# Kernel optimization log

Measured on AMD Instinct MI355X. Metric: run time of the kernel, lower is better.

## Reference

```python
import jax, jax.numpy as jnp
from jax import lax
import numpy as np

BETA = 0.9   # snn.Leaky(beta=0.9)
THR = 1.0    # snntorch default threshold, reset_mechanism='subtract'

@jax.custom_vjp
def spike(x):
    return (x > 0.0).astype(x.dtype)

def _spike_fwd(x):
    return spike(x), x

def _spike_bwd(x, g):
    # snntorch surrogate.atan (alpha=2): dS/dx = 1 / (1 + (pi*x)^2)
    return (g / (1.0 + (jnp.pi * x) ** 2),)

spike.defvjp(_spike_fwd, _spike_bwd)

def lif(inp, mem):
    # snntorch Leaky: reset based on PREVIOUS mem, detached; subtract mechanism
    reset = lax.stop_gradient(spike(mem - THR))
    mem = BETA * mem + inp - reset * THR
    return spike(mem - THR), mem

def conv1d(x, w, b):
    # x: (B, Cin, L), w: (Cout, Cin, K), VALID padding
    y = lax.conv_general_dilated(x, w, window_strides=(1,), padding='VALID',
                                 dimension_numbers=('NCH', 'OIH', 'NCH'))
    return y + b[None, :, None]

def setup_inputs() -> dict:
    key = jax.random.key(0)
    ks = jax.random.split(key, 11)
    B, L, T, num_c = 1024, 30, 100, 10
    def init(k, shape, fan_in):
        bound = 1.0 / np.sqrt(fan_in)
        return jax.random.uniform(k, shape, jnp.float32, -bound, bound)
    return {
        'x':   jax.random.normal(ks[0], (B, 1, L, T), jnp.float32),
        'w1':  init(ks[1], (16, 1, 7), 1 * 7),   'b1': init(ks[2], (16,), 7),
        'w2':  init(ks[3], (32, 16, 5), 16 * 5), 'b2': init(ks[4], (32,), 80),
        'w3':  init(ks[5], (64, 32, 3), 32 * 3), 'b3': init(ks[6], (64,), 96),
        'fw1': init(ks[7], (256, 64 * 18), 64 * 18), 'fb1': init(ks[8], (256,), 64 * 18),
        'fw2': init(ks[9], (num_c, 256), 256),       'fb2': init(ks[10], (num_c,), 256),
    }

def reference(x, w1, b1, w2, b2, w3, b3, fw1, fb1, fw2, fb2):
    B = x.shape[0]
    num_c = fw2.shape[0]
    xt_seq = jnp.transpose(x, (3, 0, 1, 2))  # (T, B, 1, 30)
    mems = (jnp.zeros((B, 16, 24), x.dtype),  # after conv1 (k=7): 30->24
            jnp.zeros((B, 32, 20), x.dtype),  # after conv2 (k=5): 24->20
            jnp.zeros((B, 64, 18), x.dtype),  # after conv3 (k=3): 20->18
            jnp.zeros((B, 256), x.dtype),
            jnp.zeros((B, num_c), x.dtype))
    def step(mems, xt):
        m1, m2, m3, m4, m5 = mems
        h = conv1d(xt, w1, b1); s, m1 = lif(h, m1)
        h = conv1d(s, w2, b2);  s, m2 = lif(h, m2)
        h = conv1d(s, w3, b3);  s, m3 = lif(h, m3)
        h = s.reshape(B, -1) @ fw1.T + fb1; s, m4 = lif(h, m4)
        h = s @ fw2.T + fb2;               s, m5 = lif(h, m5)
        return (m1, m2, m3, m4, m5), s
    _, spk_rec = lax.scan(step, mems, xt_seq)
    return spk_rec  # (T, B, num_c) -- matches torch.stack(spk_rec)
```

## Files before the change

kernel.cpp:

```cpp
#include <hip/hip_runtime.h>
#include <stdint.h>

#define BETA 0.9f

__global__ void transpose_fw1(const float* __restrict__ A, float* __restrict__ At) {
    __shared__ float tile[32][33];
    const int i0 = blockIdx.x * 32;
    const int j0 = blockIdx.y * 32;
    const int tx = threadIdx.x, ty = threadIdx.y;
    for (int r = ty; r < 32; r += 8)
        tile[r][tx] = A[(j0 + r) * 1152 + i0 + tx];
    __syncthreads();
    for (int r = ty; r < 32; r += 8)
        At[(i0 + r) * 256 + j0 + tx] = tile[tx][r];
}

__global__ __launch_bounds__(768, 6) void snn_main(
    const float* __restrict__ x,
    const float* __restrict__ w1, const float* __restrict__ b1,
    const float* __restrict__ w2, const float* __restrict__ b2,
    const float* __restrict__ w3, const float* __restrict__ b3,
    const float* __restrict__ fw1T,
    const float* __restrict__ fb1,
    const float* __restrict__ fw2, const float* __restrict__ fb2,
    float* __restrict__ out)
{
    const int b    = blockIdx.x;
    const int tid  = threadIdx.x;
    const int e    = (tid >= 384) ? 1 : 0;
    const int tl   = tid - 384 * e;
    const int lane = tid & 63;
    const int ew   = tl >> 6;

    __shared__ float w2L[16 * 5 * 32];
    __shared__ float w3L[32 * 3 * 64];
    __shared__ float pacc[2][6][256];
    __shared__ float s1e[2][16 * 24 + 8];
    __shared__ float s4[2][256];
    __shared__ unsigned long long masks[2][18];
    __shared__ unsigned int rm1[2][2][16];
    __shared__ unsigned int cm2[2][2][20];

    const int c1 = tl & 15;
    const int l1 = tl >> 4;
    const int c2 = tl & 31;
    const int g2 = tl >> 5;
    const int l02 = (g2 < 8) ? 2 * g2 : 16 + (g2 - 8);
    const int nl2 = (g2 < 8) ? 2 : 1;
    const int c3 = lane;
    const int l03 = ew * 3;
    const unsigned wmask2 = (ew < 4)  ? (0xFFu << (4 * ew)) :
                            (ew == 4) ? 0x3F0000u :
                                        0xFC0000u;

    for (int i = tid; i < 16 * 5 * 32; i += 768) {
        const int cc = i & 31, r = i >> 5;
        w2L[i] = w2[cc * 80 + r];
    }
    for (int i = tid; i < 32 * 3 * 64; i += 768) {
        const int cc = i & 63, r = i >> 6;
        w3L[i] = w3[cc * 96 + r];
    }
    if (tl < 16) { rm1[e][0][tl] = 0u; rm1[e][1][tl] = 0u; }
    if (tl < 20) { cm2[e][0][tl] = 0u; cm2[e][1][tl] = 0u; }
    if (tl < 8)  s1e[e][384 + tl] = 0.0f;

    float w1r[7];
#pragma unroll
    for (int k = 0; k < 7; ++k) w1r[k] = w1[c1 * 7 + k];
    const float b1r = b1[c1];
    const float b2r = b2[c2];
    const float b3r = b3[c3];
    const float fb1r = (tl < 256) ? fb1[tl] : 0.0f;
    const int jf = tl >> 4, chf = tl & 15;
    const float fb2r = (tl < 160 && chf == 0) ? fb2[jf] : 0.0f;
    float fw2r[16];
    if (tl < 160) {
#pragma unroll
        for (int i = 0; i < 16; ++i) fw2r[i] = fw2[jf * 256 + i * 16 + chf];
    }

    float m1 = 0.f;
    float m2[2] = {0.f, 0.f};
    float m3[3] = {0.f, 0.f, 0.f};
    float m4 = 0.f, m5 = 0.f;

    const float* xb = x + (2 * b + e) * 3000;
    const int out_b = (2 * b + e) * 10;
    const float4* fw1Tv = reinterpret_cast<const float4*>(fw1T);

    float xr[7];
#pragma unroll
    for (int k = 0; k < 7; ++k) xr[k] = xb[(l1 + k) * 100];

    __syncthreads();

    for (int t = 0; t < 100; ++t) {
        const int pb = t & 1, pn = pb ^ 1;

        {
            float h = b1r;
#pragma unroll
            for (int k = 0; k < 7; ++k) h += xr[k] * w1r[k];
            float rs = (m1 > 1.0f) ? 1.0f : 0.0f;
            m1 = BETA * m1 + h - rs;
            float sa = (m1 > 1.0f) ? 1.0f : 0.0f;
            s1e[e][c1 * 24 + l1] = sa;
            if (sa != 0.0f) atomicOr(&rm1[e][pb][c1], 1u << l1);
            const int tt = (t < 99) ? t + 1 : 99;
#pragma unroll
            for (int k = 0; k < 7; ++k) xr[k] = xb[(l1 + k) * 100 + tt];
        }
        __syncthreads();

        {
            if (tl < 16) rm1[e][pn][tl] = 0u;
            if (tl < 20) cm2[e][pn][tl] = 0u;
            float h[2] = {b2r, b2r};
#pragma unroll
            for (int ci = 0; ci < 16; ++ci) {
                const unsigned rmv =
                    __builtin_amdgcn_readfirstlane(rm1[e][pb][ci]);
                if ((rmv & wmask2) == 0u) continue;
                float win[6];
#pragma unroll
                for (int r = 0; r < 6; ++r) win[r] = s1e[e][ci * 24 + l02 + r];
                float wk[5];
#pragma unroll
                for (int k = 0; k < 5; ++k) wk[k] = w2L[(ci * 5 + k) * 32 + c2];
#pragma unroll
                for (int li = 0; li < 2; ++li)
                    if (li < nl2)
#pragma unroll
                        for (int k = 0; k < 5; ++k) h[li] += win[li + k] * wk[k];
            }
#pragma unroll
            for (int li = 0; li < 2; ++li)
                if (li < nl2) {
                    float rs = (m2[li] > 1.0f) ? 1.0f : 0.0f;
                    m2[li] = BETA * m2[li] + h[li] - rs;
                    if (m2[li] > 1.0f) atomicOr(&cm2[e][pb][l02 + li], 1u << c2);
                }
        }
        __syncthreads();

        {
            float h[3] = {b3r, b3r, b3r};
#pragma unroll
            for (int wl = 0; wl < 5; ++wl) {
                unsigned cm = __builtin_amdgcn_readfirstlane(cm2[e][pb][l03 + wl]);
                while (cm) {
                    const int ci = (int)__builtin_ctz(cm); cm &= cm - 1;
                    const float* wp = &w3L[ci * 192 + c3];
#pragma unroll
                    for (int k = 0; k < 3; ++k) {
                        const int li = wl - k;
                        if (li >= 0 && li < 3)
                            h[li] += wp[k * 64];
                    }
                }
            }
#pragma unroll
            for (int li = 0; li < 3; ++li) {
                float rs = (m3[li] > 1.0f) ? 1.0f : 0.0f;
                m3[li] = BETA * m3[li] + h[li] - rs;
                float s = (m3[li] > 1.0f) ? 1.0f : 0.0f;
                unsigned long long mk = __ballot(s != 0.0f);
                if (lane == 0) masks[e][l03 + li] = mk;
            }
        }
        __syncthreads();

        {
            float4 acc4; acc4.x = acc4.y = acc4.z = acc4.w = 0.0f;
#pragma unroll 1
            for (int l = ew; l < 18; l += 6) {
                const unsigned* mp = (const unsigned*)&masks[e][l];
                const unsigned mlo = __builtin_amdgcn_readfirstlane(mp[0]);
                const unsigned mhi = __builtin_amdgcn_readfirstlane(mp[1]);
                unsigned long long mk = ((unsigned long long)mhi << 32) | mlo;
                while (mk) {
                    float4 f0, f1, f2, f3;
                    f0.x=f0.y=f0.z=f0.w=0.f; f1=f0; f2=f0; f3=f0;
                    int c;
                    c = (int)__builtin_ctzll(mk); mk &= mk - 1;
                    f0 = fw1Tv[(c * 18 + l) * 64 + lane];
                    if (mk) { c = (int)__builtin_ctzll(mk); mk &= mk - 1;
                              f1 = fw1Tv[(c * 18 + l) * 64 + lane]; }
                    if (mk) { c = (int)__builtin_ctzll(mk); mk &= mk - 1;
                              f2 = fw1Tv[(c * 18 + l) * 64 + lane]; }
                    if (mk) { c = (int)__builtin_ctzll(mk); mk &= mk - 1;
                              f3 = fw1Tv[(c * 18 + l) * 64 + lane]; }
                    acc4.x += f0.x; acc4.y += f0.y; acc4.z += f0.z; acc4.w += f0.w;
                    acc4.x += f1.x; acc4.y += f1.y; acc4.z += f1.z; acc4.w += f1.w;
                    acc4.x += f2.x; acc4.y += f2.y; acc4.z += f2.z; acc4.w += f2.w;
                    acc4.x += f3.x; acc4.y += f3.y; acc4.z += f3.z; acc4.w += f3.w;
                }
            }
            ((float4*)&pacc[e][ew][0])[lane] = acc4;
        }
        __syncthreads();

        if (tl < 256) {
            float acc = fb1r;
#pragma unroll
            for (int w = 0; w < 6; ++w) acc += pacc[e][w][tl];
            float rs = (m4 > 1.0f) ? 1.0f : 0.0f;
            m4 = BETA * m4 + acc - rs;
            s4[e][tl] = (m4 > 1.0f) ? 1.0f : 0.0f;
        }
        __syncthreads();

        if (tl < 160) {
            float p = 0.f;
#pragma unroll
            for (int i = 0; i < 16; ++i)
                p += s4[e][i * 16 + chf] * fw2r[i];
            p += __shfl_xor(p, 8, 16);
            p += __shfl_xor(p, 4, 16);
            p += __shfl_xor(p, 2, 16);
            p += __shfl_xor(p, 1, 16);
            if (chf == 0) {
                float h = fb2r + p;
                float rs = (m5 > 1.0f) ? 1.0f : 0.0f;
                m5 = BETA * m5 + h - rs;
                out[t * 10240 + out_b + jf] = (m5 > 1.0f) ? 1.0f : 0.0f;
            }
        }
    }
}

extern "C" void kernel_launch(void* const* d_in, const int* in_sizes, int n_in,
                              void* d_out, int out_size, void* d_ws, size_t ws_size,
                              hipStream_t stream) {
    const float* x   = (const float*)d_in[0];
    const float* w1  = (const float*)d_in[1];
    const float* b1  = (const float*)d_in[2];
    const float* w2  = (const float*)d_in[3];
    const float* b2  = (const float*)d_in[4];
    const float* w3  = (const float*)d_in[5];
    const float* b3  = (const float*)d_in[6];
    const float* fw1 = (const float*)d_in[7];
    const float* fb1 = (const float*)d_in[8];
    const float* fw2 = (const float*)d_in[9];
    const float* fb2 = (const float*)d_in[10];
    float* out  = (float*)d_out;
    float* fw1T = (float*)d_ws;

    dim3 tb(32, 8);
    dim3 tg(1152 / 32, 256 / 32);
    transpose_fw1<<<tg, tb, 0, stream>>>(fw1, fw1T);
    snn_main<<<512, 768, 0, stream>>>(x, w1, b1, w2, b2, w3, b3,
                                      fw1T, fb1, fw2, fb2, out);
}
```

Before: 674.0 us.

## Replace conv2 dense window with spike-bitmask sparse accumulation; widen fc1 gather batch

Conv2 no longer reads a shared float spike array. Each thread walks the set bits of the per-channel row bitmask in its window and adds the matching w2 weights directly, which drops the s1e buffer and its stores. The fc1 sparse gather now issues up to eight float4 loads per batch instead of four, giving more memory-level parallelism. The fc2 weights are read from global memory each step instead of being held in 16 registers, which lowers register pressure at the cost of repeated cached loads. The per-thread while loops over bits can diverge within a wave, because the readfirstlane uniform skip has been removed.

```diff
diff --git a/kernel.cpp b/kernel.cpp
--- a/kernel.cpp
+++ b/kernel.cpp
@@ -35,7 +35,6 @@
     __shared__ float w2L[16 * 5 * 32];
     __shared__ float w3L[32 * 3 * 64];
     __shared__ float pacc[2][6][256];
-    __shared__ float s1e[2][16 * 24 + 8];
     __shared__ float s4[2][256];
     __shared__ unsigned long long masks[2][18];
     __shared__ unsigned int rm1[2][2][16];
@@ -47,11 +46,9 @@
     const int g2 = tl >> 5;
     const int l02 = (g2 < 8) ? 2 * g2 : 16 + (g2 - 8);
     const int nl2 = (g2 < 8) ? 2 : 1;
+    const unsigned wsel = (g2 < 8) ? 0x3Fu : 0x1Fu;
     const int c3 = lane;
     const int l03 = ew * 3;
-    const unsigned wmask2 = (ew < 4)  ? (0xFFu << (4 * ew)) :
-                            (ew == 4) ? 0x3F0000u :
-                                        0xFC0000u;
 
     for (int i = tid; i < 16 * 5 * 32; i += 768) {
         const int cc = i & 31, r = i >> 5;
@@ -63,7 +60,6 @@
     }
     if (tl < 16) { rm1[e][0][tl] = 0u; rm1[e][1][tl] = 0u; }
     if (tl < 20) { cm2[e][0][tl] = 0u; cm2[e][1][tl] = 0u; }
-    if (tl < 8)  s1e[e][384 + tl] = 0.0f;
 
     float w1r[7];
 #pragma unroll
@@ -74,11 +70,6 @@
     const float fb1r = (tl < 256) ? fb1[tl] : 0.0f;
     const int jf = tl >> 4, chf = tl & 15;
     const float fb2r = (tl < 160 && chf == 0) ? fb2[jf] : 0.0f;
-    float fw2r[16];
-    if (tl < 160) {
-#pragma unroll
-        for (int i = 0; i < 16; ++i) fw2r[i] = fw2[jf * 256 + i * 16 + chf];
-    }
 
     float m1 = 0.f;
     float m2[2] = {0.f, 0.f};
@@ -104,9 +95,7 @@
             for (int k = 0; k < 7; ++k) h += xr[k] * w1r[k];
             float rs = (m1 > 1.0f) ? 1.0f : 0.0f;
             m1 = BETA * m1 + h - rs;
-            float sa = (m1 > 1.0f) ? 1.0f : 0.0f;
-            s1e[e][c1 * 24 + l1] = sa;
-            if (sa != 0.0f) atomicOr(&rm1[e][pb][c1], 1u << l1);
+            if (m1 > 1.0f) atomicOr(&rm1[e][pb][c1], 1u << l1);
             const int tt = (t < 99) ? t + 1 : 99;
 #pragma unroll
             for (int k = 0; k < 7; ++k) xr[k] = xb[(l1 + k) * 100 + tt];
@@ -119,20 +108,14 @@
             float h[2] = {b2r, b2r};
 #pragma unroll
             for (int ci = 0; ci < 16; ++ci) {
-                const unsigned rmv =
-                    __builtin_amdgcn_readfirstlane(rm1[e][pb][ci]);
-                if ((rmv & wmask2) == 0u) continue;
-                float win[6];
-#pragma unroll
-                for (int r = 0; r < 6; ++r) win[r] = s1e[e][ci * 24 + l02 + r];
-                float wk[5];
-#pragma unroll
-                for (int k = 0; k < 5; ++k) wk[k] = w2L[(ci * 5 + k) * 32 + c2];
-#pragma unroll
-                for (int li = 0; li < 2; ++li)
-                    if (li < nl2)
-#pragma unroll
-                        for (int k = 0; k < 5; ++k) h[li] += win[li + k] * wk[k];
+                const unsigned rmv = rm1[e][pb][ci];
+                unsigned wbits = (rmv >> l02) & wsel;
+                const float* wp = &w2L[ci * 160 + c2];
+                while (wbits) {
+                    const int p = (int)__builtin_ctz(wbits); wbits &= wbits - 1;
+                    if (p <= 4)              h[0] += wp[p * 32];
+                    if (nl2 == 2 && p >= 1)  h[1] += wp[(p - 1) * 32];
+                }
             }
 #pragma unroll
             for (int li = 0; li < 2; ++li)
@@ -180,8 +163,9 @@
                 const unsigned mhi = __builtin_amdgcn_readfirstlane(mp[1]);
                 unsigned long long mk = ((unsigned long long)mhi << 32) | mlo;
                 while (mk) {
-                    float4 f0, f1, f2, f3;
+                    float4 f0, f1, f2, f3, f4, f5, f6, f7;
                     f0.x=f0.y=f0.z=f0.w=0.f; f1=f0; f2=f0; f3=f0;
+                    f4=f0; f5=f0; f6=f0; f7=f0;
                     int c;
                     c = (int)__builtin_ctzll(mk); mk &= mk - 1;
                     f0 = fw1Tv[(c * 18 + l) * 64 + lane];
@@ -191,10 +175,22 @@
                               f2 = fw1Tv[(c * 18 + l) * 64 + lane]; }
                     if (mk) { c = (int)__builtin_ctzll(mk); mk &= mk - 1;
                               f3 = fw1Tv[(c * 18 + l) * 64 + lane]; }
+                    if (mk) { c = (int)__builtin_ctzll(mk); mk &= mk - 1;
+                              f4 = fw1Tv[(c * 18 + l) * 64 + lane]; }
+                    if (mk) { c = (int)__builtin_ctzll(mk); mk &= mk - 1;
+                              f5 = fw1Tv[(c * 18 + l) * 64 + lane]; }
+                    if (mk) { c = (int)__builtin_ctzll(mk); mk &= mk - 1;
+                              f6 = fw1Tv[(c * 18 + l) * 64 + lane]; }
+                    if (mk) { c = (int)__builtin_ctzll(mk); mk &= mk - 1;
+                              f7 = fw1Tv[(c * 18 + l) * 64 + lane]; }
                     acc4.x += f0.x; acc4.y += f0.y; acc4.z += f0.z; acc4.w += f0.w;
                     acc4.x += f1.x; acc4.y += f1.y; acc4.z += f1.z; acc4.w += f1.w;
                     acc4.x += f2.x; acc4.y += f2.y; acc4.z += f2.z; acc4.w += f2.w;
                     acc4.x += f3.x; acc4.y += f3.y; acc4.z += f3.z; acc4.w += f3.w;
+                    acc4.x += f4.x; acc4.y += f4.y; acc4.z += f4.z; acc4.w += f4.w;
+                    acc4.x += f5.x; acc4.y += f5.y; acc4.z += f5.z; acc4.w += f5.w;
+                    acc4.x += f6.x; acc4.y += f6.y; acc4.z += f6.z; acc4.w += f6.w;
+                    acc4.x += f7.x; acc4.y += f7.y; acc4.z += f7.z; acc4.w += f7.w;
                 }
             }
             ((float4*)&pacc[e][ew][0])[lane] = acc4;
@@ -212,10 +208,11 @@
         __syncthreads();
 
         if (tl < 160) {
+            const float* wrow = fw2 + jf * 256;
             float p = 0.f;
 #pragma unroll
             for (int i = 0; i < 16; ++i)
-                p += s4[e][i * 16 + chf] * fw2r[i];
+                p += s4[e][i * 16 + chf] * wrow[i * 16 + chf];
             p += __shfl_xor(p, 8, 16);
             p += __shfl_xor(p, 4, 16);
             p += __shfl_xor(p, 2, 16);
```

Measured after the change: 990.4 us. 1.47x slower.
